# Performance work log

Hardware: AMD Instinct MI355X
Metric: run time of the kernel (lower is better)

## Reference

```python
import jax, jax.numpy as jnp
import numpy as np

N = 100000
E = 1250000
H = 64


def setup_inputs() -> dict:
    key = jax.random.key(0)
    ks = jax.random.split(key, 20)
    x = jax.random.normal(ks[0], (N, 1), dtype=jnp.float32)
    edge_index = jax.random.randint(ks[1], (2, E), 0, N, dtype=jnp.int64)
    edge_attr = jax.random.uniform(ks[2], (E,), dtype=jnp.float32)
    def lin(k, fin, fout):
        s = 1.0 / np.sqrt(fin)
        kw, kb = jax.random.split(k)
        W = jax.random.uniform(kw, (fin, fout), minval=-s, maxval=s, dtype=jnp.float32)
        b = jax.random.uniform(kb, (fout,), minval=-s, maxval=s, dtype=jnp.float32)
        return W, b
    W1, b1 = lin(ks[3], 1, H)
    W2, b2 = lin(ks[4], H, H)
    W3, b3 = lin(ks[5], H, H)
    W4, b4 = lin(ks[6], H, H)
    W5, b5 = lin(ks[7], H, H)
    fW1, fb1 = lin(ks[8], H, H)
    fW2, fb2 = lin(ks[9], H, 1)
    return dict(x=x, edge_index=edge_index, edge_attr=edge_attr,
                W1=W1, b1=b1, W2=W2, b2=b2, W3=W3, b3=b3, W4=W4, b4=b4,
                W5=W5, b5=b5, fW1=fW1, fb1=fb1, fW2=fW2, fb2=fb2)


def _gcn_layer(x, W, b, src, dst, ew):
    # PyG GCNConv: x' = D^{-1/2}(A+I)D^{-1/2} x W + b (self-loops pre-appended)
    h = x @ W                                   # [N, H]
    deg = jax.ops.segment_sum(ew, dst, num_segments=N)
    dinv = jnp.where(deg > 0, jax.lax.rsqrt(deg), 0.0)
    norm = dinv[src] * ew * dinv[dst]           # [E+N]
    msg = h[src] * norm[:, None]                # [E+N, H]
    return jax.ops.segment_sum(msg, dst, num_segments=N) + b


def reference(x, edge_index, edge_attr, W1, b1, W2, b2, W3, b3, W4, b4, W5, b5, fW1, fb1, fW2, fb2):
    loops = jnp.arange(N, dtype=edge_index.dtype)
    src = jnp.concatenate([edge_index[0], loops])
    dst = jnp.concatenate([edge_index[1], loops])
    ew = jnp.concatenate([edge_attr, jnp.ones((N,), edge_attr.dtype)])
    h = jax.nn.relu(_gcn_layer(x, W1, b1, src, dst, ew))
    h = jax.nn.relu(_gcn_layer(h, W2, b2, src, dst, ew))
    h = jax.nn.relu(_gcn_layer(h, W3, b3, src, dst, ew))
    h = jax.nn.relu(_gcn_layer(h, W4, b4, src, dst, ew))
    h = jax.nn.relu(_gcn_layer(h, W5, b5, src, dst, ew))
    h = jax.nn.relu(h @ fW1 + fb1)
    return h @ fW2 + fb2
```

## Files before the change

kernel.cpp:

```cpp
#include <hip/hip_runtime.h>
#include <hip/hip_bf16.h>

#define NN 100000
#define EE 1250000

#define RL(x, l) __builtin_amdgcn_readlane((x), (l))
#define RLF(x, l) __int_as_float(__builtin_amdgcn_readlane(__float_as_int(x), (l)))

typedef __attribute__((ext_vector_type(8))) short v8s;
typedef __attribute__((ext_vector_type(4))) float v4f;
typedef __attribute__((ext_vector_type(4))) unsigned int v4u;

__device__ __forceinline__ unsigned short bf16rtn(float x) {
    unsigned u = __float_as_uint(x);
    unsigned r = u + 0x7fffu + ((u >> 16) & 1u);
    return (unsigned short)(r >> 16);
}
__device__ __forceinline__ unsigned bf16rtn2(float lo, float hi) {
    return (unsigned)bf16rtn(lo) | ((unsigned)bf16rtn(hi) << 16);
}
__device__ __forceinline__ float bflo(unsigned u) { return __uint_as_float(u << 16); }
__device__ __forceinline__ float bfhi(unsigned u) { return __uint_as_float(u & 0xffff0000u); }
__device__ __forceinline__ float bfs(unsigned short s) { return __uint_as_float((unsigned)s << 16); }


__global__ __launch_bounds__(256) void k_count(const int* __restrict__ ei,
                                               int* __restrict__ cnt,
                                               int* __restrict__ slot) {
    int e = blockIdx.x * 256 + threadIdx.x;
    if (e >= EE) return;
    int d = __builtin_nontemporal_load(&ei[EE + e]);
    int s = atomicAdd(&cnt[d], 1);
    __builtin_nontemporal_store(s, &slot[e]);
}

__global__ __launch_bounds__(256) void k_bsum(const int* __restrict__ cnt, int* __restrict__ bsum) {
    __shared__ int ls[256];
    int b = blockIdx.x, tid = threadIdx.x;
    int base = b * 1024 + tid * 4;
    int s = 0;
    #pragma unroll
    for (int j = 0; j < 4; ++j) { int g = base + j; if (g < NN) s += cnt[g]; }
    ls[tid] = s; __syncthreads();
    for (int off = 128; off > 0; off >>= 1) {
        if (tid < off) ls[tid] += ls[tid + off];
        __syncthreads();
    }
    if (tid == 0) bsum[b] = ls[0];
}

__global__ __launch_bounds__(256) void k_scan_out(const int* __restrict__ cnt,
                                                  const int* __restrict__ bsum,
                                                  int* __restrict__ rowptr) {
    __shared__ int ls[256];
    __shared__ int sbase;
    int b = blockIdx.x, tid = threadIdx.x;
    if (tid < 64) {
        int w0 = (tid < b) ? bsum[tid] : 0;
        int w1 = ((64 + tid) < b) ? bsum[64 + tid] : 0;
        int s = w0 + w1;
        #pragma unroll
        for (int m = 32; m >= 1; m >>= 1) s += __shfl_xor(s, m, 64);
        if (tid == 0) sbase = s;
    }
    int base = b * 1024 + tid * 4;
    int c[4]; int s = 0;
    #pragma unroll
    for (int j = 0; j < 4; ++j) {
        int g = base + j;
        c[j] = (g < NN) ? cnt[g] : 0;
        s += c[j];
    }
    ls[tid] = s; __syncthreads();
    for (int off = 1; off < 256; off <<= 1) {
        int v = (tid >= off) ? ls[tid - off] : 0;
        __syncthreads();
        ls[tid] += v;
        __syncthreads();
    }
    int excl = ls[tid] - s + sbase;
    #pragma unroll
    for (int j = 0; j < 4; ++j) {
        int g = base + j;
        if (g < NN) {
            rowptr[g + 1] = excl + c[j];
            excl += c[j];
        }
    }
    if (b == 0 && tid == 0) rowptr[0] = 0;
}

__global__ __launch_bounds__(256) void k_fill(const int* __restrict__ ei,
                                              const float* __restrict__ ew,
                                              const int* __restrict__ slot,
                                              const int* __restrict__ rowptr,
                                              int2* __restrict__ epair) {
    int e = blockIdx.x * 256 + threadIdx.x;
    if (e >= EE) return;
    int s = __builtin_nontemporal_load(&ei[e]);
    int d = __builtin_nontemporal_load(&ei[EE + e]);
    float w = __builtin_nontemporal_load(&ew[e]);
    int sl = __builtin_nontemporal_load(&slot[e]);
    int p = rowptr[d] + sl;
    epair[p] = make_int2(s, __float_as_int(w));
}

__global__ __launch_bounds__(256) void k_deg(const int* __restrict__ rowptr,
                                             const int2* __restrict__ epair,
                                             const float* __restrict__ x,
                                             float* __restrict__ dinv,
                                             float* __restrict__ xd) {
    int lane = threadIdx.x & 63;
    int wid  = threadIdx.x >> 6;
    int l16  = lane & 15;
    int sub  = lane >> 4;
    int node = (blockIdx.x * 4 + wid) * 4 + sub;
    if (node >= NN) return;
    int beg = rowptr[node], end = rowptr[node + 1];
    float s = 0.f;
    for (int idx = beg + l16; idx < end; idx += 16)
        s += __int_as_float(epair[idx].y);
    #pragma unroll
    for (int m = 8; m >= 1; m >>= 1) s += __shfl_xor(s, m, 64);
    if (l16 == 0) {
        float di = rsqrtf(s + 1.0f);
        dinv[node] = di;
        xd[node] = di * x[node];
    }
}

__global__ __launch_bounds__(256) void k_wpk(const float* __restrict__ Wa,
                                             const float* __restrict__ Wb,
                                             const float* __restrict__ Wc,
                                             const float* __restrict__ Wd,
                                             unsigned* __restrict__ Wf) {
    const float* W = (blockIdx.x == 0) ? Wa : (blockIdx.x == 1) ? Wb
                   : (blockIdx.x == 2) ? Wc : Wd;
    unsigned* out = Wf + blockIdx.x * 4096;
    int t = threadIdx.x;
    #pragma unroll
    for (int i = 0; i < 2; ++i) {
        int s = t * 2 + i;
        int lane = s & 63;
        int nt = (s >> 6) & 3;
        int kt = s >> 8;
        int col = nt * 16 + (lane & 15);
        int k0 = kt * 32 + (lane >> 4) * 8;
        unsigned hi[4], lo[4];
        #pragma unroll
        for (int d = 0; d < 4; ++d) {
            float w0 = W[(k0 + 2 * d) * 64 + col];
            float w1 = W[(k0 + 2 * d + 1) * 64 + col];
            unsigned short h0 = bf16rtn(w0), h1 = bf16rtn(w1);
            float r0 = w0 - bfs(h0), r1 = w1 - bfs(h1);
            hi[d] = (unsigned)h0 | ((unsigned)h1 << 16);
            lo[d] = (unsigned)bf16rtn(r0) | ((unsigned)bf16rtn(r1) << 16);
        }
        int gh = (0 * 2 + kt) * 4 + nt;
        int gl = (1 * 2 + kt) * 4 + nt;
        *(v4u*)&out[(gh * 64 + lane) * 4] = (v4u){hi[0], hi[1], hi[2], hi[3]};
        *(v4u*)&out[(gl * 64 + lane) * 4] = (v4u){lo[0], lo[1], lo[2], lo[3]};
    }
}


__global__ __launch_bounds__(256) void k_l1(
    const float* __restrict__ xd, const float* __restrict__ dinv,
    const int* __restrict__ rowptr, const int2* __restrict__ ep,
    const float* __restrict__ W1, const float* __restrict__ b1,
    const float* __restrict__ W2, unsigned short* __restrict__ Gout)
{
    __shared__ float sW[4096];
    int tid = threadIdx.x;
    #pragma unroll
    for (int i = 0; i < 16; ++i) sW[tid + i * 256] = W2[tid + i * 256];
    __syncthreads();
    int lane = tid & 63, l16 = lane & 15, sub = lane >> 4;
    int g4 = blockIdx.x * 4 + (tid >> 6);
    int nodeS = g4 * 4 + sub;
    int beg = rowptr[nodeS], end = rowptr[nodeS + 1];
    float partial = 0.f;
    for (int idx = beg + l16; idx < end; idx += 16) {
        int2 p = ep[idx];
        partial = fmaf(__int_as_float(p.y), xd[p.x], partial);
    }
    #pragma unroll
    for (int m = 8; m >= 1; m >>= 1) partial += __shfl_xor(partial, m, 64);
    float z = dinv[nodeS] * (xd[nodeS] + partial);
    float z0 = RLF(z, 0), z1 = RLF(z, 16), z2 = RLF(z, 32), z3 = RLF(z, 48);
    float w1l = W1[lane], b1l = b1[lane];
    float v0 = fmaxf(fmaf(z0, w1l, b1l), 0.f);
    float v1 = fmaxf(fmaf(z1, w1l, b1l), 0.f);
    float v2 = fmaxf(fmaf(z2, w1l, b1l), 0.f);
    float v3 = fmaxf(fmaf(z3, w1l, b1l), 0.f);
    float a0 = 0.f, a1 = 0.f, a2 = 0.f, a3 = 0.f;
    #pragma unroll
    for (int k = 0; k < 64; ++k) {
        float wk = sW[k * 64 + lane];
        a0 = fmaf(RLF(v0, k), wk, a0);
        a1 = fmaf(RLF(v1, k), wk, a1);
        a2 = fmaf(RLF(v2, k), wk, a2);
        a3 = fmaf(RLF(v3, k), wk, a3);
    }
    int n0 = g4 * 4;
    Gout[(n0 + 0) * 64 + lane] = bf16rtn(dinv[n0 + 0] * a0);
    Gout[(n0 + 1) * 64 + lane] = bf16rtn(dinv[n0 + 1] * a1);
    Gout[(n0 + 2) * 64 + lane] = bf16rtn(dinv[n0 + 2] * a2);
    Gout[(n0 + 3) * 64 + lane] = bf16rtn(dinv[n0 + 3] * a3);
}

__global__ __launch_bounds__(256) void k_gmv(
    const unsigned* __restrict__ G16, const float* __restrict__ dinv,
    const int* __restrict__ rowptr, const int2* __restrict__ ep,
    const float* __restrict__ bias, const unsigned* __restrict__ Wf,
    unsigned short* __restrict__ Gout)
{
    __shared__ __align__(16) unsigned sB[4096];
    __shared__ __align__(16) unsigned sA[4][128];
    int tid = threadIdx.x;
    #pragma unroll
    for (int i = 0; i < 4; ++i)
        ((v4u*)sB)[tid + i * 256] = ((const v4u*)Wf)[tid + i * 256];
    int lane = tid & 63;
    int wid  = tid >> 6;
    int lc   = lane & 31;
    int half = lane >> 5;
    int n0 = (blockIdx.x * 4 + wid) * 4;
    float2 bb = ((const float2*)bias)[lc];
    for (int r = 0; r < 4; ++r) {
        int node = n0 + r;
        int beg = __builtin_amdgcn_readfirstlane(rowptr[node]);
        int end = __builtin_amdgcn_readfirstlane(rowptr[node + 1]);
        float ax = 0.f, ay = 0.f;
        if (half == 0) {
            unsigned u = G16[node * 32 + lc];
            ax = bflo(u); ay = bfhi(u);
        }
        int j = beg;
        for (; j + 16 <= end; j += 16) {
            unsigned u[8]; float nv[8];
            #pragma unroll
            for (int t = 0; t < 8; ++t) {
                int2 pa = ep[j + t];
                int2 pb = ep[j + 8 + t];
                int src = half ? pb.x : pa.x;
                nv[t] = __int_as_float(half ? pb.y : pa.y);
                u[t] = G16[src * 32 + lc];
            }
            #pragma unroll
            for (int t = 0; t < 8; ++t) {
                ax = fmaf(bflo(u[t]), nv[t], ax);
                ay = fmaf(bfhi(u[t]), nv[t], ay);
            }
        }
        if (j < end) {
            unsigned u[8]; float nv[8];
            #pragma unroll
            for (int t = 0; t < 8; ++t) {
                int ia = j + t, ib = j + 8 + t;
                int2 pa = ep[ia < end ? ia : j];
                int2 pb = ep[ib < end ? ib : j];
                int src = half ? pb.x : pa.x;
                float w = __int_as_float(half ? pb.y : pa.y);
                bool v = half ? (ib < end) : (ia < end);
                nv[t] = v ? w : 0.f;
                u[t] = G16[src * 32 + lc];
            }
            #pragma unroll
            for (int t = 0; t < 8; ++t) {
                ax = fmaf(bflo(u[t]), nv[t], ax);
                ay = fmaf(bfhi(u[t]), nv[t], ay);
            }
        }
        ax += __shfl_xor(ax, 32, 64);
        ay += __shfl_xor(ay, 32, 64);
        float din = dinv[node];
        float ve = fmaxf(fmaf(din, ax, bb.x), 0.f);
        float vo = fmaxf(fmaf(din, ay, bb.y), 0.f);
        if (half == 0) sA[wid][r * 32 + lc] = bf16rtn2(ve, vo);
    }
    __syncthreads();
    int rr  = lane & 3;
    int blk = lane >> 4;
    v8s a0 = *(const v8s*)&sA[wid][rr * 32 +  0 + blk * 4];
    v8s a1 = *(const v8s*)&sA[wid][rr * 32 + 16 + blk * 4];
    v4f acc[4];
    #pragma unroll
    for (int nt = 0; nt < 4; ++nt) {
        v8s bh0 = *(const v8s*)&sB[((0 * 4 + nt) * 64 + lane) * 4];
        v8s bh1 = *(const v8s*)&sB[((1 * 4 + nt) * 64 + lane) * 4];
        v8s bl0 = *(const v8s*)&sB[((2 * 4 + nt) * 64 + lane) * 4];
        v8s bl1 = *(const v8s*)&sB[((3 * 4 + nt) * 64 + lane) * 4];
        v4f c = {0.f, 0.f, 0.f, 0.f};
        c = __builtin_amdgcn_mfma_f32_16x16x32_bf16(a0, bl0, c, 0, 0, 0);
        c = __builtin_amdgcn_mfma_f32_16x16x32_bf16(a1, bl1, c, 0, 0, 0);
        c = __builtin_amdgcn_mfma_f32_16x16x32_bf16(a0, bh0, c, 0, 0, 0);
        c = __builtin_amdgcn_mfma_f32_16x16x32_bf16(a1, bh1, c, 0, 0, 0);
        acc[nt] = c;
    }
    if (lane < 16) {
        float4 dn = *(const float4*)&dinv[n0];
        #pragma unroll
        for (int r = 0; r < 4; ++r) {
            float d = (r == 0) ? dn.x : (r == 1) ? dn.y : (r == 2) ? dn.z : dn.w;
            #pragma unroll
            for (int nt = 0; nt < 4; ++nt)
                Gout[(n0 + r) * 64 + nt * 16 + lane] = bf16rtn(d * acc[nt][r]);
        }
    }
}

__global__ __launch_bounds__(256) void k_ghead(
    const unsigned* __restrict__ G16, const float* __restrict__ dinv,
    const int* __restrict__ rowptr, const int2* __restrict__ ep,
    const float* __restrict__ b5, const unsigned* __restrict__ Wf,
    const float* __restrict__ fb1, const float* __restrict__ fW2,
    const float* __restrict__ fb2, float* __restrict__ out)
{
    __shared__ __align__(16) unsigned sB[4096];
    __shared__ __align__(16) unsigned sA[4][128];
    int tid = threadIdx.x;
    #pragma unroll
    for (int i = 0; i < 4; ++i)
        ((v4u*)sB)[tid + i * 256] = ((const v4u*)Wf)[tid + i * 256];
    int lane = tid & 63;
    int wid  = tid >> 6;
    int lc   = lane & 31;
    int half = lane >> 5;
    int n0 = (blockIdx.x * 4 + wid) * 4;
    float2 bb = ((const float2*)b5)[lc];
    int l16 = lane & 15;
    float fb1v[4], fw2v[4];
    #pragma unroll
    for (int nt = 0; nt < 4; ++nt) {
        fb1v[nt] = fb1[nt * 16 + l16];
        fw2v[nt] = fW2[nt * 16 + l16];
    }
    float fb2s = fb2[0];
    for (int r = 0; r < 4; ++r) {
        int node = n0 + r;
        int beg = __builtin_amdgcn_readfirstlane(rowptr[node]);
        int end = __builtin_amdgcn_readfirstlane(rowptr[node + 1]);
        float ax = 0.f, ay = 0.f;
        if (half == 0) {
            unsigned u = G16[node * 32 + lc];
            ax = bflo(u); ay = bfhi(u);
        }
        int j = beg;
        for (; j + 16 <= end; j += 16) {
            unsigned u[8]; float nv[8];
            #pragma unroll
            for (int t = 0; t < 8; ++t) {
                int2 pa = ep[j + t];
                int2 pb = ep[j + 8 + t];
                int src = half ? pb.x : pa.x;
                nv[t] = __int_as_float(half ? pb.y : pa.y);
                u[t] = G16[src * 32 + lc];
            }
            #pragma unroll
            for (int t = 0; t < 8; ++t) {
                ax = fmaf(bflo(u[t]), nv[t], ax);
                ay = fmaf(bfhi(u[t]), nv[t], ay);
            }
        }
        if (j < end) {
            unsigned u[8]; float nv[8];
            #pragma unroll
            for (int t = 0; t < 8; ++t) {
                int ia = j + t, ib = j + 8 + t;
                int2 pa = ep[ia < end ? ia : j];
                int2 pb = ep[ib < end ? ib : j];
                int src = half ? pb.x : pa.x;
                float w = __int_as_float(half ? pb.y : pa.y);
                bool v = half ? (ib < end) : (ia < end);
                nv[t] = v ? w : 0.f;
                u[t] = G16[src * 32 + lc];
            }
            #pragma unroll
            for (int t = 0; t < 8; ++t) {
                ax = fmaf(bflo(u[t]), nv[t], ax);
                ay = fmaf(bfhi(u[t]), nv[t], ay);
            }
        }
        ax += __shfl_xor(ax, 32, 64);
        ay += __shfl_xor(ay, 32, 64);
        float din = dinv[node];
        float ve = fmaxf(fmaf(din, ax, bb.x), 0.f);
        float vo = fmaxf(fmaf(din, ay, bb.y), 0.f);
        if (half == 0) sA[wid][r * 32 + lc] = bf16rtn2(ve, vo);
    }
    __syncthreads();
    int rr  = lane & 3;
    int blk = lane >> 4;
    v8s a0 = *(const v8s*)&sA[wid][rr * 32 +  0 + blk * 4];
    v8s a1 = *(const v8s*)&sA[wid][rr * 32 + 16 + blk * 4];
    v4f acc[4];
    #pragma unroll
    for (int nt = 0; nt < 4; ++nt) {
        v8s bh0 = *(const v8s*)&sB[((0 * 4 + nt) * 64 + lane) * 4];
        v8s bh1 = *(const v8s*)&sB[((1 * 4 + nt) * 64 + lane) * 4];
        v8s bl0 = *(const v8s*)&sB[((2 * 4 + nt) * 64 + lane) * 4];
        v8s bl1 = *(const v8s*)&sB[((3 * 4 + nt) * 64 + lane) * 4];
        v4f c = {0.f, 0.f, 0.f, 0.f};
        c = __builtin_amdgcn_mfma_f32_16x16x32_bf16(a0, bl0, c, 0, 0, 0);
        c = __builtin_amdgcn_mfma_f32_16x16x32_bf16(a1, bl1, c, 0, 0, 0);
        c = __builtin_amdgcn_mfma_f32_16x16x32_bf16(a0, bh0, c, 0, 0, 0);
        c = __builtin_amdgcn_mfma_f32_16x16x32_bf16(a1, bh1, c, 0, 0, 0);
        acc[nt] = c;
    }
    float tr[4];
    #pragma unroll
    for (int r = 0; r < 4; ++r) {
        float t = 0.f;
        #pragma unroll
        for (int nt = 0; nt < 4; ++nt)
            t += fmaxf(acc[nt][r] + fb1v[nt], 0.f) * fw2v[nt];
        #pragma unroll
        for (int m = 8; m >= 1; m >>= 1) t += __shfl_xor(t, m, 64);
        tr[r] = t;
    }
    if (lane == 0) {
        float4 o = {tr[0] + fb2s, tr[1] + fb2s, tr[2] + fb2s, tr[3] + fb2s};
        *(float4*)&out[n0] = o;
    }
}


extern "C" void kernel_launch(void* const* d_in, const int* in_sizes, int n_in,
                              void* d_out, int out_size, void* d_ws, size_t ws_size,
                              hipStream_t stream) {
    const float* x   = (const float*)d_in[0];
    const int*   ei  = (const int*)d_in[1];
    const float* ew  = (const float*)d_in[2];
    const float* W1  = (const float*)d_in[3];
    const float* b1  = (const float*)d_in[4];
    const float* W2  = (const float*)d_in[5];
    const float* b2  = (const float*)d_in[6];
    const float* W3  = (const float*)d_in[7];
    const float* b3  = (const float*)d_in[8];
    const float* W4  = (const float*)d_in[9];
    const float* b4  = (const float*)d_in[10];
    const float* W5  = (const float*)d_in[11];
    const float* b5  = (const float*)d_in[12];
    const float* fW1 = (const float*)d_in[13];
    const float* fb1 = (const float*)d_in[14];
    const float* fW2 = (const float*)d_in[15];
    const float* fb2 = (const float*)d_in[16];
    float* out = (float*)d_out;

    char* ws = (char*)d_ws;
    size_t o = 0;
    auto alloc = [&](size_t elems) -> void* {
        void* p = (void*)(ws + o);
        o += ((elems * 4 + 255) / 256) * 256;
        return p;
    };
    float* dinv   = (float*)alloc(NN);
    float* xd     = (float*)alloc(NN);
    int*   rowptr = (int*)alloc(NN + 1);
    int*   cnt    = (int*)alloc(NN);
    int*   bsum   = (int*)alloc(128);
    int2*  epair  = (int2*)alloc(2 * (size_t)EE);
    unsigned* Ga16 = (unsigned*)alloc((size_t)NN * 32);
    unsigned* Gb16 = (unsigned*)alloc((size_t)NN * 32);
    int*   slot   = (int*)alloc(EE);
    unsigned* Wf  = (unsigned*)alloc(4 * 4096);

    int gE  = (EE + 255) / 256;
    int nb  = (NN + 1023) / 1024;
    int gW4 = NN / 16;

    k_wpk<<<4, 256, 0, stream>>>(W3, W4, W5, fW1, Wf);
    hipMemsetAsync(cnt, 0, NN * sizeof(int), stream);
    k_count<<<gE, 256, 0, stream>>>(ei, cnt, slot);
    k_bsum<<<nb, 256, 0, stream>>>(cnt, bsum);
    k_scan_out<<<nb, 256, 0, stream>>>(cnt, bsum, rowptr);
    k_fill<<<gE, 256, 0, stream>>>(ei, ew, slot, rowptr, epair);
    k_deg<<<gW4, 256, 0, stream>>>(rowptr, epair, x, dinv, xd);

    k_l1<<<gW4, 256, 0, stream>>>(xd, dinv, rowptr, epair, W1, b1, W2,
                                  (unsigned short*)Ga16);
    k_gmv<<<gW4, 256, 0, stream>>>(Ga16, dinv, rowptr, epair, b2, Wf + 0,
                                   (unsigned short*)Gb16);
    k_gmv<<<gW4, 256, 0, stream>>>(Gb16, dinv, rowptr, epair, b3, Wf + 4096,
                                   (unsigned short*)Ga16);
    k_gmv<<<gW4, 256, 0, stream>>>(Ga16, dinv, rowptr, epair, b4, Wf + 8192,
                                   (unsigned short*)Gb16);
    k_ghead<<<gW4, 256, 0, stream>>>(Gb16, dinv, rowptr, epair, b5, Wf + 12288,
                                     fb1, fW2, fb2, out);
}
```

Before: 427.1 us.

## Fuse degree accumulation into count atomics via packed 64-bit fixed-point add

The edge count and the weighted degree sum are packed into one 64-bit atomic: the high 32 bits hold the count and the low 32 bits hold the edge weight in 24-bit fixed point. The scan kernel then computes dinv and xd directly, so the separate k_deg kernel, which re-read the whole CSR edge array, is removed. This trades one extra weight load and 64-bit atomics in k_count for one fewer kernel launch and one fewer pass over the edges. Fixed-point quantization adds a small degree error, and the low word could overflow into the count if a node's weight sum reached 256.

```diff
diff --git a/kernel.cpp b/kernel.cpp
--- a/kernel.cpp
+++ b/kernel.cpp
@@ -25,22 +25,27 @@
 
 
 __global__ __launch_bounds__(256) void k_count(const int* __restrict__ ei,
-                                               int* __restrict__ cnt,
+                                               const float* __restrict__ ew,
+                                               unsigned long long* __restrict__ cnt,
                                                int* __restrict__ slot) {
     int e = blockIdx.x * 256 + threadIdx.x;
     if (e >= EE) return;
     int d = __builtin_nontemporal_load(&ei[EE + e]);
-    int s = atomicAdd(&cnt[d], 1);
-    __builtin_nontemporal_store(s, &slot[e]);
-}
-
-__global__ __launch_bounds__(256) void k_bsum(const int* __restrict__ cnt, int* __restrict__ bsum) {
+    float w = __builtin_nontemporal_load(&ew[e]);
+    unsigned fx = (unsigned)(w * 16777216.0f + 0.5f);
+    unsigned long long old =
+        atomicAdd(&cnt[d], (1ULL << 32) | (unsigned long long)fx);
+    __builtin_nontemporal_store((int)(old >> 32), &slot[e]);
+}
+
+__global__ __launch_bounds__(256) void k_bsum(const unsigned long long* __restrict__ cnt,
+                                              int* __restrict__ bsum) {
     __shared__ int ls[256];
     int b = blockIdx.x, tid = threadIdx.x;
     int base = b * 1024 + tid * 4;
     int s = 0;
     #pragma unroll
-    for (int j = 0; j < 4; ++j) { int g = base + j; if (g < NN) s += cnt[g]; }
+    for (int j = 0; j < 4; ++j) { int g = base + j; if (g < NN) s += (int)(cnt[g] >> 32); }
     ls[tid] = s; __syncthreads();
     for (int off = 128; off > 0; off >>= 1) {
         if (tid < off) ls[tid] += ls[tid + off];
@@ -49,9 +54,12 @@
     if (tid == 0) bsum[b] = ls[0];
 }
 
-__global__ __launch_bounds__(256) void k_scan_out(const int* __restrict__ cnt,
+__global__ __launch_bounds__(256) void k_scan_out(const unsigned long long* __restrict__ cnt,
                                                   const int* __restrict__ bsum,
-                                                  int* __restrict__ rowptr) {
+                                                  const float* __restrict__ x,
+                                                  int* __restrict__ rowptr,
+                                                  float* __restrict__ dinv,
+                                                  float* __restrict__ xd) {
     __shared__ int ls[256];
     __shared__ int sbase;
     int b = blockIdx.x, tid = threadIdx.x;
@@ -64,11 +72,13 @@
         if (tid == 0) sbase = s;
     }
     int base = b * 1024 + tid * 4;
-    int c[4]; int s = 0;
+    int c[4]; float sw[4]; int s = 0;
     #pragma unroll
     for (int j = 0; j < 4; ++j) {
         int g = base + j;
-        c[j] = (g < NN) ? cnt[g] : 0;
+        unsigned long long v = (g < NN) ? cnt[g] : 0ULL;
+        c[j] = (int)(v >> 32);
+        sw[j] = (float)(unsigned)(v & 0xffffffffu) * (1.0f / 16777216.0f);
         s += c[j];
     }
     ls[tid] = s; __syncthreads();
@@ -85,6 +95,9 @@
         if (g < NN) {
             rowptr[g + 1] = excl + c[j];
             excl += c[j];
+            float di = rsqrtf(sw[j] + 1.0f);
+            dinv[g] = di;
+            xd[g] = di * x[g];
         }
     }
     if (b == 0 && tid == 0) rowptr[0] = 0;
@@ -103,30 +116,6 @@
     int sl = __builtin_nontemporal_load(&slot[e]);
     int p = rowptr[d] + sl;
     epair[p] = make_int2(s, __float_as_int(w));
-}
-
-__global__ __launch_bounds__(256) void k_deg(const int* __restrict__ rowptr,
-                                             const int2* __restrict__ epair,
-                                             const float* __restrict__ x,
-                                             float* __restrict__ dinv,
-                                             float* __restrict__ xd) {
-    int lane = threadIdx.x & 63;
-    int wid  = threadIdx.x >> 6;
-    int l16  = lane & 15;
-    int sub  = lane >> 4;
-    int node = (blockIdx.x * 4 + wid) * 4 + sub;
-    if (node >= NN) return;
-    int beg = rowptr[node], end = rowptr[node + 1];
-    float s = 0.f;
-    for (int idx = beg + l16; idx < end; idx += 16)
-        s += __int_as_float(epair[idx].y);
-    #pragma unroll
-    for (int m = 8; m >= 1; m >>= 1) s += __shfl_xor(s, m, 64);
-    if (l16 == 0) {
-        float di = rsqrtf(s + 1.0f);
-        dinv[node] = di;
-        xd[node] = di * x[node];
-    }
 }
 
 __global__ __launch_bounds__(256) void k_wpk(const float* __restrict__ Wa,
@@ -458,7 +447,7 @@
     float* dinv   = (float*)alloc(NN);
     float* xd     = (float*)alloc(NN);
     int*   rowptr = (int*)alloc(NN + 1);
-    int*   cnt    = (int*)alloc(NN);
+    unsigned long long* cnt64 = (unsigned long long*)alloc(2 * (size_t)NN);
     int*   bsum   = (int*)alloc(128);
     int2*  epair  = (int2*)alloc(2 * (size_t)EE);
     unsigned* Ga16 = (unsigned*)alloc((size_t)NN * 32);
@@ -471,12 +460,11 @@
     int gW4 = NN / 16;
 
     k_wpk<<<4, 256, 0, stream>>>(W3, W4, W5, fW1, Wf);
-    hipMemsetAsync(cnt, 0, NN * sizeof(int), stream);
-    k_count<<<gE, 256, 0, stream>>>(ei, cnt, slot);
-    k_bsum<<<nb, 256, 0, stream>>>(cnt, bsum);
-    k_scan_out<<<nb, 256, 0, stream>>>(cnt, bsum, rowptr);
+    hipMemsetAsync(cnt64, 0, NN * sizeof(unsigned long long), stream);
+    k_count<<<gE, 256, 0, stream>>>(ei, ew, cnt64, slot);
+    k_bsum<<<nb, 256, 0, stream>>>(cnt64, bsum);
+    k_scan_out<<<nb, 256, 0, stream>>>(cnt64, bsum, x, rowptr, dinv, xd);
     k_fill<<<gE, 256, 0, stream>>>(ei, ew, slot, rowptr, epair);
-    k_deg<<<gW4, 256, 0, stream>>>(rowptr, epair, x, dinv, xd);
 
     k_l1<<<gW4, 256, 0, stream>>>(xd, dinv, rowptr, epair, W1, b1, W2,
                                   (unsigned short*)Ga16);
```

After: 428.0 us. No clear change (+0.2%).
